# Kernel tuning notes

Measured on AMD Instinct MI355X. Metric: run time of the kernel, lower is better.

Reference implementation:

```python
import jax, jax.numpy as jnp
import numpy as np
import math

B, C, N = 16, 512, 2048
MID = C // 2
EPS = 1e-5

def setup_inputs() -> dict:
    key = jax.random.key(0)
    ks = jax.random.split(key, 16)
    s = 0.02
    return {
        "x": jax.random.normal(ks[0], (B, C, N), jnp.float32),
        "wq": jax.random.normal(ks[1], (MID, C), jnp.float32) * s,
        "bq": jnp.zeros((MID,), jnp.float32),
        "gq": jnp.ones((MID,), jnp.float32),
        "betaq": jnp.zeros((MID,), jnp.float32),
        "wk": jax.random.normal(ks[2], (MID, C), jnp.float32) * s,
        "bk": jnp.zeros((MID,), jnp.float32),
        "gk": jnp.ones((MID,), jnp.float32),
        "betak": jnp.zeros((MID,), jnp.float32),
        "wv": jax.random.normal(ks[3], (MID, C), jnp.float32) * s,
        "bv": jnp.zeros((MID,), jnp.float32),
        "wo": jax.random.normal(ks[4], (C, MID), jnp.float32) * s,
        "bo": jnp.zeros((C,), jnp.float32),
        "mq": jnp.zeros((MID,), jnp.float32),
        "vq": jnp.ones((MID,), jnp.float32),
        "mk": jnp.zeros((MID,), jnp.float32),
        "vk": jnp.ones((MID,), jnp.float32),
    }

def _proj(x, w, b):
    # 1x1 Conv1d == per-position linear: [mid, C] x [B, C, N] -> [B, mid, N]
    return jnp.einsum('mc,bcn->bmn', w, x) + b[None, :, None]

def _bn_relu(z, gamma, beta, mean, var):
    # eval-mode BatchNorm1d over channel axis, then ReLU
    inv = gamma / jnp.sqrt(var + EPS)
    return jax.nn.relu(z * inv[None, :, None] + (beta - mean * inv)[None, :, None])

def reference(x, wq, bq, gq, betaq, wk, bk, gk, betak, wv, bv, wo, bo, mq, vq, mk, vk):
    q = _bn_relu(_proj(x, wq, bq), gq, betaq, mq, vq)   # [B, mid, N]
    k = _bn_relu(_proj(x, wk, bk), gk, betak, mk, vk)   # [B, mid, N]
    v = _proj(x, wv, bv)                                # [B, mid, N]
    scores = jnp.einsum('bmi,bmj->bij', q, k) / math.sqrt(MID)  # [B, Nq, Nk]
    attn = jax.nn.softmax(scores, axis=1)               # softmax over QUERY axis (dim=1)
    ctx = jnp.einsum('bci,bij->bcj', v, attn)           # [B, mid, N]
    out = jnp.einsum('cm,bmn->bcn', wo, ctx) + bo[None, :, None]
    return x + out
```

## Files before the change

kernel.cpp:

```cpp
#include <hip/hip_runtime.h>
#include <hip/hip_bf16.h>

#define B_ 16
#define C_ 512
#define N_ 2048
#define MID_ 256
#define EPS_ 1e-5f

typedef __attribute__((ext_vector_type(8))) short bf16x8;
typedef __attribute__((ext_vector_type(4))) float f32x4;
typedef __attribute__((ext_vector_type(8))) unsigned short us8;
typedef __attribute__((ext_vector_type(4))) unsigned short us4;

static __device__ __forceinline__ float bf2f(unsigned short u) {
    union { unsigned int i; float f; } c; c.i = ((unsigned int)u) << 16; return c.f;
}
static __device__ __forceinline__ unsigned short f2bf(float f) {
    __hip_bfloat16 h = __float2bfloat16(f);
    return *reinterpret_cast<unsigned short*>(&h);
}
static __device__ __forceinline__ us8 pack8(float4 a, float4 b) {
    us8 r;
    r[0] = f2bf(a.x); r[1] = f2bf(a.y); r[2] = f2bf(a.z); r[3] = f2bf(a.w);
    r[4] = f2bf(b.x); r[5] = f2bf(b.y); r[6] = f2bf(b.z); r[7] = f2bf(b.w);
    return r;
}

__global__ __launch_bounds__(256) void prep_x_kernel(
    const float* __restrict__ x, unsigned short* __restrict__ xt)
{
    const int b  = blockIdx.z;
    const int c0 = blockIdx.y * 64;
    const int n0 = blockIdx.x * 64;
    __shared__ unsigned short Ts[64][72];

    const int tid = threadIdx.x;
    const int cc  = tid >> 2;
    const int cq  = (tid & 3) * 4;

    #pragma unroll
    for (int i = 0; i < 4; i++) {
        float4 f = *(const float4*)&x[((size_t)b * C_ + c0 + cc) * N_ + n0 + cq + 16 * i];
        Ts[cq + 16 * i + 0][cc] = f2bf(f.x);
        Ts[cq + 16 * i + 1][cc] = f2bf(f.y);
        Ts[cq + 16 * i + 2][cc] = f2bf(f.z);
        Ts[cq + 16 * i + 3][cc] = f2bf(f.w);
    }
    __syncthreads();

    const int nn = tid >> 2;
    const int cg = (tid & 3) * 16;
    #pragma unroll
    for (int i = 0; i < 2; i++)
        *(us8*)&xt[((size_t)b * N_ + n0 + nn) * C_ + c0 + cg + 8 * i] =
            *(const us8*)&Ts[nn][cg + 8 * i];
}

__global__ __launch_bounds__(256) void prep_w_kernel(
    const float* __restrict__ wq, const float* __restrict__ wk,
    const float* __restrict__ wv, unsigned short* __restrict__ wb)
{
    const int nthr = gridDim.x * 256;
    for (int u = blockIdx.x * 256 + threadIdx.x; u < 98304; u += nthr) {
        int p = u >> 15;
        int o4 = u & 32767;
        const float* src = (p == 0) ? wq : (p == 1) ? wk : wv;
        float4 f = *(const float4*)&src[o4 * 4];
        us4 r;
        r[0] = f2bf(f.x); r[1] = f2bf(f.y); r[2] = f2bf(f.z); r[3] = f2bf(f.w);
        *(us4*)&wb[(size_t)p * 131072 + o4 * 4] = r;
    }
}

__global__ __launch_bounds__(256) void qkv_gemm_kernel(
    const unsigned short* __restrict__ xt, const unsigned short* __restrict__ wb,
    const float* __restrict__ bq, const float* __restrict__ gq,
    const float* __restrict__ betaq, const float* __restrict__ mq,
    const float* __restrict__ vq,
    const float* __restrict__ bk, const float* __restrict__ gk,
    const float* __restrict__ betak, const float* __restrict__ mk,
    const float* __restrict__ vk,
    const float* __restrict__ bv,
    unsigned short* __restrict__ qt, unsigned short* __restrict__ kt,
    unsigned short* __restrict__ v)
{
    const int p  = blockIdx.z % 3;
    const int b  = blockIdx.z / 3;
    const int n0 = blockIdx.x * 128;
    const int m0 = blockIdx.y * 128;

    __shared__ unsigned short Ws[128][72];
    __shared__ unsigned short Xs[128][72];
    __shared__ float sc_s[128], of_s[128];

    const int tid  = threadIdx.x;
    const int wave = tid >> 6;
    const int lane = tid & 63;
    const int quad = lane >> 4;
    const int l16  = lane & 15;
    const int wi   = wave >> 1;
    const int wj   = wave & 1;

    const unsigned short* wbp = wb + (size_t)p * 131072;
    const unsigned short* xtb = xt + (size_t)b * N_ * C_;

    if (tid < 128) {
        int m = m0 + tid;
        if (p == 0) {
            float inv = gq[m] * rsqrtf(vq[m] + EPS_);
            sc_s[tid] = inv * 0.0625f;
            of_s[tid] = ((bq[m] - mq[m]) * inv + betaq[m]) * 0.0625f;
        } else if (p == 1) {
            float inv = gk[m] * rsqrtf(vk[m] + EPS_);
            sc_s[tid] = inv; of_s[tid] = (bk[m] - mk[m]) * inv + betak[m];
        } else {
            sc_s[tid] = 1.0f; of_s[tid] = bv[m];
        }
    }

    unsigned short (*Asrc)[72] = (p == 2) ? Xs : Ws;
    unsigned short (*Bsrc)[72] = (p == 2) ? Ws : Xs;

    f32x4 acc[4][4];
    #pragma unroll
    for (int it = 0; it < 4; it++)
        #pragma unroll
        for (int jt = 0; jt < 4; jt++)
            #pragma unroll
            for (int r = 0; r < 4; r++) acc[it][jt][r] = 0.0f;

    const int srow  = tid >> 1;
    const int shalf = (tid & 1) * 32;

    for (int k0 = 0; k0 < C_; k0 += 64) {
        __syncthreads();
        #pragma unroll
        for (int i = 0; i < 4; i++) {
            *(us8*)&Ws[srow][shalf + 8 * i] =
                *(const us8*)&wbp[(size_t)(m0 + srow) * C_ + k0 + shalf + 8 * i];
            *(us8*)&Xs[srow][shalf + 8 * i] =
                *(const us8*)&xtb[(size_t)(n0 + srow) * C_ + k0 + shalf + 8 * i];
        }
        __syncthreads();
        #pragma unroll
        for (int cl = 0; cl < 64; cl += 32) {
            bf16x8 af[4], bfr[4];
            #pragma unroll
            for (int t = 0; t < 4; t++)
                af[t] = *(const bf16x8*)&Asrc[wi * 64 + t * 16 + l16][cl + quad * 8];
            #pragma unroll
            for (int t = 0; t < 4; t++)
                bfr[t] = *(const bf16x8*)&Bsrc[wj * 64 + t * 16 + l16][cl + quad * 8];
            #pragma unroll
            for (int it = 0; it < 4; it++)
                #pragma unroll
                for (int jt = 0; jt < 4; jt++)
                    acc[it][jt] = __builtin_amdgcn_mfma_f32_16x16x32_bf16(
                        af[it], bfr[jt], acc[it][jt], 0, 0, 0);
        }
    }
    __syncthreads();

    if (p < 2) {
        unsigned short* outT = (p == 0) ? qt : kt;
        #pragma unroll
        for (int it = 0; it < 4; it++) {
            int ml = wi * 64 + it * 16 + quad * 4;
            #pragma unroll
            for (int jt = 0; jt < 4; jt++) {
                int n = n0 + wj * 64 + jt * 16 + l16;
                us4 pk;
                #pragma unroll
                for (int r = 0; r < 4; r++) {
                    float val = acc[it][jt][r] * sc_s[ml + r] + of_s[ml + r];
                    pk[r] = f2bf(fmaxf(val, 0.0f));
                }
                *(us4*)&outT[((size_t)b * N_ + n) * MID_ + m0 + ml] = pk;
            }
        }
    } else {
        #pragma unroll
        for (int it = 0; it < 4; it++) {
            int nl = n0 + wi * 64 + it * 16 + quad * 4;
            #pragma unroll
            for (int jt = 0; jt < 4; jt++) {
                int mloc = wj * 64 + jt * 16 + l16;
                float off = of_s[mloc];
                us4 pk;
                #pragma unroll
                for (int r = 0; r < 4; r++)
                    pk[r] = f2bf(acc[it][jt][r] + off);
                *(us4*)&v[((size_t)b * MID_ + m0 + mloc) * N_ + nl] = pk;
            }
        }
    }
}

__global__ __launch_bounds__(256, 2) void flash_kernel(
    const unsigned short* __restrict__ qt,
    const unsigned short* __restrict__ kt,
    const unsigned short* __restrict__ v,
    unsigned short* __restrict__ ctxT)
{
    const int b  = blockIdx.y;
    const int j0 = blockIdx.x * 64;

    __shared__ unsigned short Ks[64][264];
    __shared__ unsigned short Ps[2][64][72];
    __shared__ float red[4][64];

    const int tid  = threadIdx.x;
    const int wave = tid >> 6;
    const int lane = tid & 63;
    const int quad = lane >> 4;
    const int l16  = lane & 15;

    const unsigned short* qb = qt + (size_t)b * N_ * MID_;
    const unsigned short* kb = kt + (size_t)b * N_ * MID_;
    const unsigned short* vb = v  + (size_t)b * MID_ * N_;

    #pragma unroll
    for (int r = 0; r < 8; r++) {
        int ch = tid + r * 256;
        int j = ch >> 5, c8 = ch & 31;
        *(us8*)&Ks[j][c8 * 8] = *(const us8*)&kb[(size_t)(j0 + j) * MID_ + c8 * 8];
    }
    __syncthreads();

    bf16x8 kc[2][8];
    #pragma unroll
    for (int jt = 0; jt < 2; jt++)
        #pragma unroll
        for (int c = 0; c < 8; c++)
            kc[jt][c] = *(const bf16x8*)&Ks[jt * 16 + l16][c * 32 + quad * 8];

    f32x4 O[4][4];
    #pragma unroll
    for (int ct = 0; ct < 4; ct++)
        #pragma unroll
        for (int jt = 0; jt < 4; jt++)
            #pragma unroll
            for (int r = 0; r < 4; r++) O[ct][jt][r] = 0.0f;
    float psum[4] = {0.0f, 0.0f, 0.0f, 0.0f};

    const unsigned short* qbase = qb + (size_t)(wave * 16 + l16) * MID_ + quad * 8;
    const unsigned short* vbase = vb + (size_t)(wave * 64 + l16) * N_ + quad * 8;

    {
        f32x4 S[4];
        #pragma unroll
        for (int jt = 0; jt < 4; jt++)
            #pragma unroll
            for (int r = 0; r < 4; r++) S[jt][r] = 0.0f;

        #pragma unroll
        for (int c = 0; c < 8; c++) {
            bf16x8 a = *(const bf16x8*)(qbase + c * 32);
            S[0] = __builtin_amdgcn_mfma_f32_16x16x32_bf16(a, kc[0][c], S[0], 0, 0, 0);
            S[1] = __builtin_amdgcn_mfma_f32_16x16x32_bf16(a, kc[1][c], S[1], 0, 0, 0);
            bf16x8 b2 = *(const bf16x8*)&Ks[32 + l16][c * 32 + quad * 8];
            S[2] = __builtin_amdgcn_mfma_f32_16x16x32_bf16(a, b2, S[2], 0, 0, 0);
            bf16x8 b3 = *(const bf16x8*)&Ks[48 + l16][c * 32 + quad * 8];
            S[3] = __builtin_amdgcn_mfma_f32_16x16x32_bf16(a, b3, S[3], 0, 0, 0);
        }
        #pragma unroll
        for (int jt = 0; jt < 4; jt++) {
            us4 pk;
            #pragma unroll
            for (int r = 0; r < 4; r++) {
                float e = __expf(S[jt][r]);
                psum[jt] += e;
                pk[r] = f2bf(e);
            }
            *(us4*)&Ps[0][jt * 16 + l16][wave * 16 + quad * 4] = pk;
        }
    }
    __syncthreads();

    for (int t = 0; t < 31; t++) {
        const int i0  = t * 64;
        const int buf = t & 1;

        #pragma unroll
        for (int ic = 0; ic < 64; ic += 32) {
            bf16x8 pb[4];
            #pragma unroll
            for (int jt = 0; jt < 4; jt++)
                pb[jt] = *(const bf16x8*)&Ps[buf][jt * 16 + l16][ic + quad * 8];
            #pragma unroll
            for (int ct = 0; ct < 4; ct++) {
                bf16x8 av = *(const bf16x8*)(vbase + (size_t)(ct * 16) * N_ + i0 + ic);
                #pragma unroll
                for (int jt = 0; jt < 4; jt++)
                    O[ct][jt] = __builtin_amdgcn_mfma_f32_16x16x32_bf16(
                        av, pb[jt], O[ct][jt], 0, 0, 0);
            }
        }

        f32x4 S[4];
        #pragma unroll
        for (int jt = 0; jt < 4; jt++)
            #pragma unroll
            for (int r = 0; r < 4; r++) S[jt][r] = 0.0f;

        const unsigned short* qp = qbase + (size_t)(i0 + 64) * MID_;
        #pragma unroll
        for (int c = 0; c < 8; c++) {
            bf16x8 a = *(const bf16x8*)(qp + c * 32);
            S[0] = __builtin_amdgcn_mfma_f32_16x16x32_bf16(a, kc[0][c], S[0], 0, 0, 0);
            S[1] = __builtin_amdgcn_mfma_f32_16x16x32_bf16(a, kc[1][c], S[1], 0, 0, 0);
            bf16x8 b2 = *(const bf16x8*)&Ks[32 + l16][c * 32 + quad * 8];
            S[2] = __builtin_amdgcn_mfma_f32_16x16x32_bf16(a, b2, S[2], 0, 0, 0);
            bf16x8 b3 = *(const bf16x8*)&Ks[48 + l16][c * 32 + quad * 8];
            S[3] = __builtin_amdgcn_mfma_f32_16x16x32_bf16(a, b3, S[3], 0, 0, 0);
        }

        #pragma unroll
        for (int jt = 0; jt < 4; jt++) {
            us4 pk;
            #pragma unroll
            for (int r = 0; r < 4; r++) {
                float e = __expf(S[jt][r]);
                psum[jt] += e;
                pk[r] = f2bf(e);
            }
            *(us4*)&Ps[buf ^ 1][jt * 16 + l16][wave * 16 + quad * 4] = pk;
        }
        __syncthreads();
    }

    {
        const int i0 = 31 * 64;
        #pragma unroll
        for (int ic = 0; ic < 64; ic += 32) {
            bf16x8 pb[4];
            #pragma unroll
            for (int jt = 0; jt < 4; jt++)
                pb[jt] = *(const bf16x8*)&Ps[31 & 1][jt * 16 + l16][ic + quad * 8];
            #pragma unroll
            for (int ct = 0; ct < 4; ct++) {
                bf16x8 av = *(const bf16x8*)(vbase + (size_t)(ct * 16) * N_ + i0 + ic);
                #pragma unroll
                for (int jt = 0; jt < 4; jt++)
                    O[ct][jt] = __builtin_amdgcn_mfma_f32_16x16x32_bf16(
                        av, pb[jt], O[ct][jt], 0, 0, 0);
            }
        }
    }

    #pragma unroll
    for (int jt = 0; jt < 4; jt++) {
        psum[jt] += __shfl_xor(psum[jt], 16, 64);
        psum[jt] += __shfl_xor(psum[jt], 32, 64);
    }
    __syncthreads();
    if (quad == 0)
        #pragma unroll
        for (int jt = 0; jt < 4; jt++) red[wave][jt * 16 + l16] = psum[jt];
    __syncthreads();

    float rl[4];
    #pragma unroll
    for (int jt = 0; jt < 4; jt++)
        rl[jt] = 1.0f / (red[0][jt * 16 + l16] + red[1][jt * 16 + l16] +
                         red[2][jt * 16 + l16] + red[3][jt * 16 + l16]);

    #pragma unroll
    for (int ct = 0; ct < 4; ct++) {
        #pragma unroll
        for (int jt = 0; jt < 4; jt++) {
            us4 pk;
            #pragma unroll
            for (int r = 0; r < 4; r++)
                pk[r] = f2bf(O[ct][jt][r] * rl[jt]);
            int j = j0 + jt * 16 + l16;
            *(us4*)&ctxT[((size_t)b * N_ + j) * MID_ + wave * 64 + ct * 16 + quad * 4] = pk;
        }
    }
}

__global__ __launch_bounds__(256) void out_gemm_kernel(
    const float* __restrict__ wo, const float* __restrict__ bo,
    const unsigned short* __restrict__ ctxT, const float* __restrict__ x,
    float* __restrict__ out)
{
    const int b   = blockIdx.z;
    const int n0  = blockIdx.x * 128;
    const int co0 = blockIdx.y * 128;

    __shared__ unsigned short Wos[128][72];
    __shared__ unsigned short Cs[128][72];
    __shared__ float bo_s[128];

    const int tid  = threadIdx.x;
    const int wave = tid >> 6;
    const int lane = tid & 63;
    const int quad = lane >> 4;
    const int l16  = lane & 15;
    const int wi   = wave >> 1;
    const int wj   = wave & 1;

    if (tid < 128) bo_s[tid] = bo[co0 + tid];

    f32x4 acc[4][4];
    #pragma unroll
    for (int it = 0; it < 4; it++)
        #pragma unroll
        for (int jt = 0; jt < 4; jt++)
            #pragma unroll
            for (int r = 0; r < 4; r++) acc[it][jt][r] = 0.0f;

    const int srow  = tid >> 1;
    const int shalf = (tid & 1) * 32;

    for (int k0 = 0; k0 < MID_; k0 += 64) {
        __syncthreads();
        #pragma unroll
        for (int i = 0; i < 4; i++) {
            float4 f0 = *(const float4*)&wo[(size_t)(co0 + srow) * MID_ + k0 + shalf + 8 * i];
            float4 f1 = *(const float4*)&wo[(size_t)(co0 + srow) * MID_ + k0 + shalf + 8 * i + 4];
            *(us8*)&Wos[srow][shalf + 8 * i] = pack8(f0, f1);
            *(us8*)&Cs[srow][shalf + 8 * i] =
                *(const us8*)&ctxT[((size_t)b * N_ + n0 + srow) * MID_ + k0 + shalf + 8 * i];
        }
        __syncthreads();
        #pragma unroll
        for (int cl = 0; cl < 64; cl += 32) {
            bf16x8 af[4], bfr[4];
            #pragma unroll
            for (int t = 0; t < 4; t++)
                af[t] = *(const bf16x8*)&Wos[wi * 64 + t * 16 + l16][cl + quad * 8];
            #pragma unroll
            for (int t = 0; t < 4; t++)
                bfr[t] = *(const bf16x8*)&Cs[wj * 64 + t * 16 + l16][cl + quad * 8];
            #pragma unroll
            for (int it = 0; it < 4; it++)
                #pragma unroll
                for (int jt = 0; jt < 4; jt++)
                    acc[it][jt] = __builtin_amdgcn_mfma_f32_16x16x32_bf16(
                        af[it], bfr[jt], acc[it][jt], 0, 0, 0);
        }
    }
    __syncthreads();

    #pragma unroll
    for (int it = 0; it < 4; it++) {
        #pragma unroll
        for (int r = 0; r < 4; r++) {
            int col = wi * 64 + it * 16 + quad * 4 + r;
            int co = co0 + col;
            float bias = bo_s[col];
            #pragma unroll
            for (int jt = 0; jt < 4; jt++) {
                int n = n0 + wj * 64 + jt * 16 + l16;
                size_t a = ((size_t)b * C_ + co) * N_ + n;
                out[a] = acc[it][jt][r] + bias + x[a];
            }
        }
    }
}

extern "C" void kernel_launch(void* const* d_in, const int* in_sizes, int n_in,
                              void* d_out, int out_size, void* d_ws, size_t ws_size,
                              hipStream_t stream) {
    const float* x     = (const float*)d_in[0];
    const float* wq    = (const float*)d_in[1];
    const float* bq    = (const float*)d_in[2];
    const float* gq    = (const float*)d_in[3];
    const float* betaq = (const float*)d_in[4];
    const float* wk    = (const float*)d_in[5];
    const float* bk    = (const float*)d_in[6];
    const float* gk    = (const float*)d_in[7];
    const float* betak = (const float*)d_in[8];
    const float* wv    = (const float*)d_in[9];
    const float* bv    = (const float*)d_in[10];
    const float* wo    = (const float*)d_in[11];
    const float* bo    = (const float*)d_in[12];
    const float* mq    = (const float*)d_in[13];
    const float* vq    = (const float*)d_in[14];
    const float* mk    = (const float*)d_in[15];
    const float* vk    = (const float*)d_in[16];
    float* out = (float*)d_out;

    const size_t elems = (size_t)B_ * MID_ * N_;
    unsigned short* qt   = (unsigned short*)d_ws;
    unsigned short* kt   = qt + elems;
    unsigned short* v    = kt + elems;
    unsigned short* ctxT = v + elems;

    unsigned short* xt = (unsigned short*)d_out;
    unsigned short* wb = xt + (size_t)B_ * N_ * C_;

    prep_x_kernel<<<dim3(N_ / 64, C_ / 64, B_), 256, 0, stream>>>(x, xt);
    prep_w_kernel<<<dim3(96), 256, 0, stream>>>(wq, wk, wv, wb);

    qkv_gemm_kernel<<<dim3(N_ / 128, MID_ / 128, B_ * 3), 256, 0, stream>>>(
        xt, wb, bq, gq, betaq, mq, vq, bk, gk, betak, mk, vk, bv, qt, kt, v);

    flash_kernel<<<dim3(N_ / 64, B_), 256, 0, stream>>>(qt, kt, v, ctxT);

    out_gemm_kernel<<<dim3(N_ / 128, C_ / 128, B_), 256, 0, stream>>>(
        wo, bo, ctxT, x, out);
}
```

Baseline: 381.3 us.

## Double flash kernel waves to 8, split MID across waves, process 128 queries per step

The flash attention kernel now launches 512 threads (8 waves) per block. Each wave owns 32 of the MID channels for the P·V accumulation instead of 64, so accumulator registers are halved. The query step widens from 64 to 128 rows, which halves the number of block barriers. The K fragments that were cached in registers are now reread from LDS, and V fragments are batch-loaded before the MFMAs. This is meant to raise occupancy and latency hiding, at the cost of more LDS traffic and a larger Ps buffer.

Result: faster. 369.9 us (-3.0%).

```diff
diff --git a/kernel.cpp b/kernel.cpp
--- a/kernel.cpp
+++ b/kernel.cpp
@@ -196,7 +196,7 @@
     }
 }
 
-__global__ __launch_bounds__(256, 2) void flash_kernel(
+__global__ __launch_bounds__(512, 4) void flash_kernel(
     const unsigned short* __restrict__ qt,
     const unsigned short* __restrict__ kt,
     const unsigned short* __restrict__ v,
@@ -206,8 +206,8 @@
     const int j0 = blockIdx.x * 64;
 
     __shared__ unsigned short Ks[64][264];
-    __shared__ unsigned short Ps[2][64][72];
-    __shared__ float red[4][64];
+    __shared__ unsigned short Ps[2][64][136];
+    __shared__ float red[8][64];
 
     const int tid  = threadIdx.x;
     const int wave = tid >> 6;
@@ -220,23 +220,16 @@
     const unsigned short* vb = v  + (size_t)b * MID_ * N_;
 
     #pragma unroll
-    for (int r = 0; r < 8; r++) {
-        int ch = tid + r * 256;
+    for (int r = 0; r < 4; r++) {
+        int ch = tid + r * 512;
         int j = ch >> 5, c8 = ch & 31;
         *(us8*)&Ks[j][c8 * 8] = *(const us8*)&kb[(size_t)(j0 + j) * MID_ + c8 * 8];
     }
     __syncthreads();
 
-    bf16x8 kc[2][8];
-    #pragma unroll
-    for (int jt = 0; jt < 2; jt++)
-        #pragma unroll
-        for (int c = 0; c < 8; c++)
-            kc[jt][c] = *(const bf16x8*)&Ks[jt * 16 + l16][c * 32 + quad * 8];
-
-    f32x4 O[4][4];
-    #pragma unroll
-    for (int ct = 0; ct < 4; ct++)
+    f32x4 O[2][4];
+    #pragma unroll
+    for (int ct = 0; ct < 2; ct++)
         #pragma unroll
         for (int jt = 0; jt < 4; jt++)
             #pragma unroll
@@ -244,7 +237,7 @@
     float psum[4] = {0.0f, 0.0f, 0.0f, 0.0f};
 
     const unsigned short* qbase = qb + (size_t)(wave * 16 + l16) * MID_ + quad * 8;
-    const unsigned short* vbase = vb + (size_t)(wave * 64 + l16) * N_ + quad * 8;
+    const unsigned short* vbase = vb + (size_t)(wave * 32 + l16) * N_ + quad * 8;
 
     {
         f32x4 S[4];
@@ -253,15 +246,17 @@
             #pragma unroll
             for (int r = 0; r < 4; r++) S[jt][r] = 0.0f;
 
+        bf16x8 qf[8];
+        #pragma unroll
+        for (int c = 0; c < 8; c++)
+            qf[c] = *(const bf16x8*)(qbase + c * 32);
         #pragma unroll
         for (int c = 0; c < 8; c++) {
-            bf16x8 a = *(const bf16x8*)(qbase + c * 32);
-            S[0] = __builtin_amdgcn_mfma_f32_16x16x32_bf16(a, kc[0][c], S[0], 0, 0, 0);
-            S[1] = __builtin_amdgcn_mfma_f32_16x16x32_bf16(a, kc[1][c], S[1], 0, 0, 0);
-            bf16x8 b2 = *(const bf16x8*)&Ks[32 + l16][c * 32 + quad * 8];
-            S[2] = __builtin_amdgcn_mfma_f32_16x16x32_bf16(a, b2, S[2], 0, 0, 0);
-            bf16x8 b3 = *(const bf16x8*)&Ks[48 + l16][c * 32 + quad * 8];
-            S[3] = __builtin_amdgcn_mfma_f32_16x16x32_bf16(a, b3, S[3], 0, 0, 0);
+            #pragma unroll
+            for (int jt = 0; jt < 4; jt++) {
+                bf16x8 bfr = *(const bf16x8*)&Ks[jt * 16 + l16][c * 32 + quad * 8];
+                S[jt] = __builtin_amdgcn_mfma_f32_16x16x32_bf16(qf[c], bfr, S[jt], 0, 0, 0);
+            }
         }
         #pragma unroll
         for (int jt = 0; jt < 4; jt++) {
@@ -277,74 +272,85 @@
     }
     __syncthreads();
 
-    for (int t = 0; t < 31; t++) {
-        const int i0  = t * 64;
+    for (int t = 0; t < 15; t++) {
+        const int i0  = t * 128;
         const int buf = t & 1;
 
-        #pragma unroll
-        for (int ic = 0; ic < 64; ic += 32) {
+        {
+            f32x4 S[4];
+            #pragma unroll
+            for (int jt = 0; jt < 4; jt++)
+                #pragma unroll
+                for (int r = 0; r < 4; r++) S[jt][r] = 0.0f;
+
+            const unsigned short* qp = qbase + (size_t)(i0 + 128) * MID_;
+            bf16x8 qf[8];
+            #pragma unroll
+            for (int c = 0; c < 8; c++)
+                qf[c] = *(const bf16x8*)(qp + c * 32);
+            #pragma unroll
+            for (int c = 0; c < 8; c++) {
+                #pragma unroll
+                for (int jt = 0; jt < 4; jt++) {
+                    bf16x8 bfr = *(const bf16x8*)&Ks[jt * 16 + l16][c * 32 + quad * 8];
+                    S[jt] = __builtin_amdgcn_mfma_f32_16x16x32_bf16(qf[c], bfr, S[jt], 0, 0, 0);
+                }
+            }
+            #pragma unroll
+            for (int jt = 0; jt < 4; jt++) {
+                us4 pk;
+                #pragma unroll
+                for (int r = 0; r < 4; r++) {
+                    float e = __expf(S[jt][r]);
+                    psum[jt] += e;
+                    pk[r] = f2bf(e);
+                }
+                *(us4*)&Ps[buf ^ 1][jt * 16 + l16][wave * 16 + quad * 4] = pk;
+            }
+        }
+
+        {
+            bf16x8 av[8];
+            #pragma unroll
+            for (int u = 0; u < 8; u++)
+                av[u] = *(const bf16x8*)(vbase + (size_t)((u >> 2) * 16) * N_ +
+                                         i0 + (u & 3) * 32);
+            #pragma unroll
+            for (int ic = 0; ic < 128; ic += 32) {
+                bf16x8 pb[4];
+                #pragma unroll
+                for (int jt = 0; jt < 4; jt++)
+                    pb[jt] = *(const bf16x8*)&Ps[buf][jt * 16 + l16][ic + quad * 8];
+                #pragma unroll
+                for (int ct = 0; ct < 2; ct++)
+                    #pragma unroll
+                    for (int jt = 0; jt < 4; jt++)
+                        O[ct][jt] = __builtin_amdgcn_mfma_f32_16x16x32_bf16(
+                            av[ct * 4 + (ic >> 5)], pb[jt], O[ct][jt], 0, 0, 0);
+            }
+        }
+        __syncthreads();
+    }
+
+    {
+        const int i0 = 15 * 128;
+        bf16x8 av[8];
+        #pragma unroll
+        for (int u = 0; u < 8; u++)
+            av[u] = *(const bf16x8*)(vbase + (size_t)((u >> 2) * 16) * N_ +
+                                     i0 + (u & 3) * 32);
+        #pragma unroll
+        for (int ic = 0; ic < 128; ic += 32) {
             bf16x8 pb[4];
             #pragma unroll
             for (int jt = 0; jt < 4; jt++)
-                pb[jt] = *(const bf16x8*)&Ps[buf][jt * 16 + l16][ic + quad * 8];
-            #pragma unroll
-            for (int ct = 0; ct < 4; ct++) {
-                bf16x8 av = *(const bf16x8*)(vbase + (size_t)(ct * 16) * N_ + i0 + ic);
+                pb[jt] = *(const bf16x8*)&Ps[1][jt * 16 + l16][ic + quad * 8];
+            #pragma unroll
+            for (int ct = 0; ct < 2; ct++)
                 #pragma unroll
                 for (int jt = 0; jt < 4; jt++)
                     O[ct][jt] = __builtin_amdgcn_mfma_f32_16x16x32_bf16(
-                        av, pb[jt], O[ct][jt], 0, 0, 0);
-            }
-        }
-
-        f32x4 S[4];
-        #pragma unroll
-        for (int jt = 0; jt < 4; jt++)
-            #pragma unroll
-            for (int r = 0; r < 4; r++) S[jt][r] = 0.0f;
-
-        const unsigned short* qp = qbase + (size_t)(i0 + 64) * MID_;
-        #pragma unroll
-        for (int c = 0; c < 8; c++) {
-            bf16x8 a = *(const bf16x8*)(qp + c * 32);
-            S[0] = __builtin_amdgcn_mfma_f32_16x16x32_bf16(a, kc[0][c], S[0], 0, 0, 0);
-            S[1] = __builtin_amdgcn_mfma_f32_16x16x32_bf16(a, kc[1][c], S[1], 0, 0, 0);
-            bf16x8 b2 = *(const bf16x8*)&Ks[32 + l16][c * 32 + quad * 8];
-            S[2] = __builtin_amdgcn_mfma_f32_16x16x32_bf16(a, b2, S[2], 0, 0, 0);
-            bf16x8 b3 = *(const bf16x8*)&Ks[48 + l16][c * 32 + quad * 8];
-            S[3] = __builtin_amdgcn_mfma_f32_16x16x32_bf16(a, b3, S[3], 0, 0, 0);
-        }
-
-        #pragma unroll
-        for (int jt = 0; jt < 4; jt++) {
-            us4 pk;
-            #pragma unroll
-            for (int r = 0; r < 4; r++) {
-                float e = __expf(S[jt][r]);
-                psum[jt] += e;
-                pk[r] = f2bf(e);
-            }
-            *(us4*)&Ps[buf ^ 1][jt * 16 + l16][wave * 16 + quad * 4] = pk;
-        }
-        __syncthreads();
-    }
-
-    {
-        const int i0 = 31 * 64;
-        #pragma unroll
-        for (int ic = 0; ic < 64; ic += 32) {
-            bf16x8 pb[4];
-            #pragma unroll
-            for (int jt = 0; jt < 4; jt++)
-                pb[jt] = *(const bf16x8*)&Ps[31 & 1][jt * 16 + l16][ic + quad * 8];
-            #pragma unroll
-            for (int ct = 0; ct < 4; ct++) {
-                bf16x8 av = *(const bf16x8*)(vbase + (size_t)(ct * 16) * N_ + i0 + ic);
-                #pragma unroll
-                for (int jt = 0; jt < 4; jt++)
-                    O[ct][jt] = __builtin_amdgcn_mfma_f32_16x16x32_bf16(
-                        av, pb[jt], O[ct][jt], 0, 0, 0);
-            }
+                        av[ct * 4 + (ic >> 5)], pb[jt], O[ct][jt], 0, 0, 0);
         }
     }
 
@@ -361,12 +367,15 @@
 
     float rl[4];
     #pragma unroll
-    for (int jt = 0; jt < 4; jt++)
-        rl[jt] = 1.0f / (red[0][jt * 16 + l16] + red[1][jt * 16 + l16] +
-                         red[2][jt * 16 + l16] + red[3][jt * 16 + l16]);
-
-    #pragma unroll
-    for (int ct = 0; ct < 4; ct++) {
+    for (int jt = 0; jt < 4; jt++) {
+        float s = 0.0f;
+        #pragma unroll
+        for (int w = 0; w < 8; w++) s += red[w][jt * 16 + l16];
+        rl[jt] = 1.0f / s;
+    }
+
+    #pragma unroll
+    for (int ct = 0; ct < 2; ct++) {
         #pragma unroll
         for (int jt = 0; jt < 4; jt++) {
             us4 pk;
@@ -374,7 +383,7 @@
             for (int r = 0; r < 4; r++)
                 pk[r] = f2bf(O[ct][jt][r] * rl[jt]);
             int j = j0 + jt * 16 + l16;
-            *(us4*)&ctxT[((size_t)b * N_ + j) * MID_ + wave * 64 + ct * 16 + quad * 4] = pk;
+            *(us4*)&ctxT[((size_t)b * N_ + j) * MID_ + wave * 32 + ct * 16 + quad * 4] = pk;
         }
     }
 }
@@ -497,7 +506,7 @@
     qkv_gemm_kernel<<<dim3(N_ / 128, MID_ / 128, B_ * 3), 256, 0, stream>>>(
         xt, wb, bq, gq, betaq, mq, vq, bk, gk, betak, mk, vk, bv, qt, kt, v);
 
-    flash_kernel<<<dim3(N_ / 64, B_), 256, 0, stream>>>(qt, kt, v, ctxT);
+    flash_kernel<<<dim3(N_ / 64, B_), 512, 0, stream>>>(qt, kt, v, ctxT);
 
     out_gemm_kernel<<<dim3(N_ / 128, C_ / 128, B_), 256, 0, stream>>>(
         wo, bo, ctxT, x, out);
```
